# Optimization experiments

Measured on AMD Instinct MI355X. Metric: run time of the kernel, lower is better.

The kernel has to match this reference:

```python
import jax, jax.numpy as jnp
import numpy as np

B, T, E = 2, 2048, 1024
H, D = 16, 64          # num_heads, head_dim (v_head_dim == head_dim)


def setup_inputs() -> dict:
    key = jax.random.key(0)
    ks = jax.random.split(key, 10)
    s = lambda fan_in: 1.0 / np.sqrt(fan_in)
    inp = {
        "embed": jax.random.normal(ks[0], (B, T, E), dtype=jnp.float32),
        "mask": jax.random.randint(ks[1], (B, T, T), 0, 2) > 0,
        # Linear weights stored as [in, out] (y = x @ W + b)
        "Wq": jax.random.uniform(ks[2], (E, H * D), minval=-s(E), maxval=s(E)),
        "bq": jnp.zeros((H * D,), jnp.float32),
        "Wk": jax.random.uniform(ks[3], (E, H * D), minval=-s(E), maxval=s(E)),
        "bk": jnp.zeros((H * D,), jnp.float32),
        "Wv": jax.random.uniform(ks[4], (E, H * D), minval=-s(E), maxval=s(E)),
        "bv": jnp.zeros((H * D,), jnp.float32),
        "Wz": jax.random.uniform(ks[5], (H * D, E), minval=-s(H * D), maxval=s(H * D)),
        "bz": jnp.zeros((E,), jnp.float32),
    }
    return inp


def reference(embed, mask, Wq, bq, Wk, bk, Wv, bv, Wz, bz):
    # Self-attention: context = embed
    q = (embed @ Wq + bq).reshape(B, T, H, D)   # b t h d
    k = (embed @ Wk + bk).reshape(B, T, H, D)   # b T h d
    v = (embed @ Wv + bv).reshape(B, T, H, D)   # b T h d

    scale = D ** (-0.5)
    score = jnp.einsum('bthd,bThd->bhtT', q, k) * scale   # [b,h,t,T] materialized, as in source
    max_neg = -jnp.finfo(score.dtype).max
    score = jnp.where(mask[:, None, :, :], score, max_neg)
    norm_score = jax.nn.softmax(score, axis=-1)
    z = jnp.einsum('bhtT,bThd->bthd', norm_score, v)      # [b,t,h,d]
    flat_z = z.reshape(B, T, H * D)
    return flat_z @ Wz + bz
```

## Files before the change

kernel.cpp:

```cpp
#include <hip/hip_runtime.h>
#include <hip/hip_bf16.h>


typedef __bf16 bf8_t  __attribute__((ext_vector_type(8)));
typedef __bf16 bf4_t  __attribute__((ext_vector_type(4)));
typedef float  f4_t   __attribute__((ext_vector_type(4)));

constexpr int Bb = 2, Tt = 2048, Hh = 16, Dd = 64;

#define ASYNC16(g, l)                                                        \
    __builtin_amdgcn_global_load_lds(                                        \
        (const __attribute__((address_space(1))) void*)(g),                  \
        (__attribute__((address_space(3))) void*)(l), 16, 0, 0)

#if __has_builtin(__builtin_amdgcn_exp2f)
#define EXP2F(x) __builtin_amdgcn_exp2f(x)
#else
#define EXP2F(x) exp2f(x)
#endif

__global__ __launch_bounds__(256) void convert_kernel(
    const float* __restrict__ in, __bf16* __restrict__ out)
{
    int i = (blockIdx.x * 256 + threadIdx.x) * 4;
    float4 v = *reinterpret_cast<const float4*>(in + i);
    bf4_t o = {(__bf16)v.x, (__bf16)v.y, (__bf16)v.z, (__bf16)v.w};
    *reinterpret_cast<bf4_t*>(out + i) = o;
}

__global__ __launch_bounds__(256) void transpose_kernel(
    const float* __restrict__ w0, const float* __restrict__ w1,
    const float* __restrict__ w2, const float* __restrict__ w3,
    __bf16* __restrict__ o0, __bf16* __restrict__ o1,
    __bf16* __restrict__ o2, __bf16* __restrict__ o3)
{
    const float* in; __bf16* out;
    switch (blockIdx.z) {
        case 0: in = w0; out = o0; break;
        case 1: in = w1; out = o1; break;
        case 2: in = w2; out = o2; break;
        default: in = w3; out = o3; break;
    }
    __shared__ float t[32][33];
    int x  = threadIdx.x & 31;
    int y0 = threadIdx.x >> 5;
    int bx = blockIdx.x * 32;
    int by = blockIdx.y * 32;
    #pragma unroll
    for (int i = 0; i < 4; i++) {
        int y = y0 + i * 8;
        t[y][x] = in[(size_t)(by + y) * 1024 + bx + x];
    }
    __syncthreads();
    #pragma unroll
    for (int i = 0; i < 4; i++) {
        int y = y0 + i * 8;
        out[(size_t)(bx + y) * 1024 + by + x] = (__bf16)t[x][y];
    }
}

template <int TM, typename OutT>
__device__ __forceinline__ void gemm_body(const __bf16* __restrict__ A,
                                          const __bf16* __restrict__ Bt,
                                          const float* __restrict__ bias,
                                          OutT* __restrict__ out,
                                          int mode, float oscale, int bx, int by)
{
    constexpr int NI = TM / 32;
    alignas(16) __shared__ __bf16 As[TM * 64];
    alignas(16) __shared__ __bf16 Bs[128 * 64];

    int tid  = threadIdx.x;
    int lane = tid & 63;
    int quad = lane >> 4;
    int l16  = lane & 15;
    int wave = tid >> 6;
    int wm   = wave >> 1, wn = wave & 1;

    f4_t acc[NI][4];
    #pragma unroll
    for (int i = 0; i < NI; i++)
        #pragma unroll
        for (int j = 0; j < 4; j++)
            acc[i][j] = f4_t{0.f, 0.f, 0.f, 0.f};

    for (int kt = 0; kt < 1024; kt += 64) {
        #pragma unroll
        for (int i = 0; i < TM / 32; i++) {
            int c   = tid + 256 * i;
            int row = c >> 3, j = c & 7;
            ASYNC16(A + (size_t)(by * TM + row) * 1024 + kt + ((j ^ (row & 7)) * 8),
                    &As[c * 8]);
        }
        #pragma unroll
        for (int i = 0; i < 4; i++) {
            int c   = tid + 256 * i;
            int row = c >> 3, j = c & 7;
            ASYNC16(Bt + (size_t)(bx * 128 + row) * 1024 + kt + ((j ^ (row & 7)) * 8),
                    &Bs[c * 8]);
        }
        __syncthreads();

        bf8_t af[2][NI], bfr[2][4];
        #pragma unroll
        for (int c = 0; c < 2; c++) {
            #pragma unroll
            for (int im = 0; im < NI; im++) {
                int row = wm * (TM / 2) + im * 16 + l16;
                af[c][im] = *reinterpret_cast<const bf8_t*>(
                    &As[row * 64 + (((c * 4 + quad) ^ (row & 7)) * 8)]);
            }
            #pragma unroll
            for (int in_ = 0; in_ < 4; in_++) {
                int row = wn * 64 + in_ * 16 + l16;
                bfr[c][in_] = *reinterpret_cast<const bf8_t*>(
                    &Bs[row * 64 + (((c * 4 + quad) ^ (row & 7)) * 8)]);
            }
        }
        #pragma unroll
        for (int c = 0; c < 2; c++)
            #pragma unroll
            for (int im = 0; im < NI; im++)
                #pragma unroll
                for (int in_ = 0; in_ < 4; in_++)
                    acc[im][in_] = __builtin_amdgcn_mfma_f32_16x16x32_bf16(
                        af[c][im], bfr[c][in_], acc[im][in_], 0, 0, 0);
        __syncthreads();
    }

    #pragma unroll
    for (int im = 0; im < NI; im++) {
        #pragma unroll
        for (int in_ = 0; in_ < 4; in_++) {
            int gc  = bx * 128 + wn * 64 + in_ * 16 + l16;
            float bb = bias[gc];
            int gr0 = by * TM + wm * (TM / 2) + im * 16 + quad * 4;
            if (mode == 2) {
                int b = gr0 >> 11, t0 = gr0 & 2047;
                int h = gc >> 6,  d = gc & 63;
                bf4_t ov;
                #pragma unroll
                for (int r = 0; r < 4; r++)
                    ov[r] = (__bf16)(acc[im][in_][r] + bb);
                *reinterpret_cast<bf4_t*>(
                    (__bf16*)out + ((size_t)(b * Hh + h) * Dd + d) * Tt + t0) = ov;
            } else {
                #pragma unroll
                for (int r = 0; r < 4; r++) {
                    int gr  = gr0 + r;
                    float v = (acc[im][in_][r] + bb) * oscale;
                    size_t idx;
                    if (mode == 0) {
                        idx = (size_t)gr * 1024 + gc;
                    } else {
                        int b = gr >> 11, t = gr & 2047;
                        int h = gc >> 6,  d = gc & 63;
                        idx = ((size_t)(b * Hh + h) * Tt + t) * Dd + d;
                    }
                    out[idx] = (OutT)v;
                }
            }
        }
    }
}

__global__ __launch_bounds__(256) void gemm_qkv_kernel(
    const __bf16* __restrict__ A,
    const __bf16* __restrict__ WqT, const __bf16* __restrict__ WkT, const __bf16* __restrict__ WvT,
    const float* __restrict__ bq,  const float* __restrict__ bk,  const float* __restrict__ bv,
    __bf16* __restrict__ Qo, __bf16* __restrict__ Ko, __bf16* __restrict__ Vo)
{
    const __bf16* Bt; const float* bias; __bf16* out; int mode; float sc;
    if      (blockIdx.z == 0) { Bt = WqT; bias = bq; out = Qo; mode = 1; sc = 0.18033688011112042f; }
    else if (blockIdx.z == 1) { Bt = WkT; bias = bk; out = Ko; mode = 1; sc = 1.f; }
    else                      { Bt = WvT; bias = bv; out = Vo; mode = 2; sc = 1.f; }
    gemm_body<128, __bf16>(A, Bt, bias, out, mode, sc, blockIdx.x, blockIdx.y);
}

__global__ __launch_bounds__(256) void gemm_out_kernel(
    const __bf16* __restrict__ A, const __bf16* __restrict__ Bt,
    const float* __restrict__ bias, float* __restrict__ out)
{
    gemm_body<64, float>(A, Bt, bias, out, 0, 1.f, blockIdx.x, blockIdx.y);
}

__global__ __launch_bounds__(512, 4) void flash_kernel(
    const __bf16* __restrict__ Qb, const __bf16* __restrict__ Kb,
    const __bf16* __restrict__ Vb, const int* __restrict__ mask,
    __bf16* __restrict__ Zb)
{
    alignas(16) __shared__ __bf16 Ks[2][64 * 64];
    alignas(16) __shared__ __bf16 Vs[2][64 * 64];
    alignas(16) __shared__ __bf16 Ps[8 * 16 * 72];

    int tid  = threadIdx.x;
    int lane = tid & 63;
    int wave = tid >> 6;
    int quad = lane >> 4;
    int l16  = lane & 15;
    int b = blockIdx.z, h = blockIdx.y;
    int bh = b * Hh + h;
    int qrow = blockIdx.x * 128 + wave * 16;

    int srow = tid >> 3, sj = tid & 7;
    const __bf16* kgp = Kb + ((size_t)bh * Tt + srow) * Dd + ((sj ^ (srow & 7)) * 8);
    const __bf16* vgp = Vb + ((size_t)bh * Dd + srow) * Tt + ((sj ^ (srow & 7)) * 8);
    const int sdst = tid * 8;

    bf8_t qf[2];
    #pragma unroll
    for (int c = 0; c < 2; c++)
        qf[c] = *reinterpret_cast<const bf8_t*>(
            Qb + ((size_t)bh * Tt + qrow + l16) * Dd + c * 32 + quad * 8);

    const int* mp = mask + ((size_t)b * Tt + qrow + l16) * Tt + quad * 4;

    float l_i = 0.f;
    f4_t o[4];
    #pragma unroll
    for (int d = 0; d < 4; d++) o[d] = f4_t{0.f, 0.f, 0.f, 0.f};

    __bf16* pw = Ps + wave * 16 * 72;

    bf8_t kreg = *reinterpret_cast<const bf8_t*>(kgp);
    bf8_t vreg = *reinterpret_cast<const bf8_t*>(vgp);
    int4 ireg[4];
    #pragma unroll
    for (int n = 0; n < 4; n++)
        ireg[n] = *reinterpret_cast<const int4*>(mp + n * 16);

    for (int kt = 0; kt < Tt; kt += 64) {
        int par = (kt >> 6) & 1;
        *reinterpret_cast<bf8_t*>(&Ks[par][sdst]) = kreg;
        *reinterpret_cast<bf8_t*>(&Vs[par][sdst]) = vreg;
        f4_t s[4];
        #pragma unroll
        for (int n = 0; n < 4; n++)
            s[n] = f4_t{ireg[n].x ? 0.f : -1e30f, ireg[n].y ? 0.f : -1e30f,
                        ireg[n].z ? 0.f : -1e30f, ireg[n].w ? 0.f : -1e30f};
        __syncthreads();

        int ktn = (kt + 64 < Tt) ? kt + 64 : 0;
        kreg = *reinterpret_cast<const bf8_t*>(kgp + (size_t)ktn * Dd);
        vreg = *reinterpret_cast<const bf8_t*>(vgp + ktn);
        #pragma unroll
        for (int n = 0; n < 4; n++)
            ireg[n] = *reinterpret_cast<const int4*>(mp + ktn + n * 16);

        #pragma unroll
        for (int c = 0; c < 2; c++)
            #pragma unroll
            for (int n = 0; n < 4; n++) {
                int krow = n * 16 + l16;
                bf8_t kf = *reinterpret_cast<const bf8_t*>(
                    &Ks[par][krow * 64 + (((c * 4 + quad) ^ (krow & 7)) * 8)]);
                s[n] = __builtin_amdgcn_mfma_f32_16x16x32_bf16(kf, qf[c], s[n], 0, 0, 0);
            }

        float rs = 0.f;
        #pragma unroll
        for (int n = 0; n < 4; n++) {
            bf4_t pv4;
            #pragma unroll
            for (int r = 0; r < 4; r++) {
                float p = EXP2F(s[n][r]);
                rs += p;
                pv4[r] = (__bf16)p;
            }
            *reinterpret_cast<bf4_t*>(&pw[l16 * 72 + n * 16 + quad * 4]) = pv4;
        }
        rs += __shfl_xor(rs, 16);
        rs += __shfl_xor(rs, 32);
        l_i += rs;

        #pragma unroll
        for (int c = 0; c < 2; c++) {
            bf8_t pf = *reinterpret_cast<const bf8_t*>(
                &pw[l16 * 72 + c * 32 + quad * 8]);
            #pragma unroll
            for (int ds = 0; ds < 4; ds++) {
                int vrow = ds * 16 + l16;
                bf8_t vf = *reinterpret_cast<const bf8_t*>(
                    &Vs[par][vrow * 64 + (((c * 4 + quad) ^ (vrow & 7)) * 8)]);
                o[ds] = __builtin_amdgcn_mfma_f32_16x16x32_bf16(vf, pf, o[ds], 0, 0, 0);
            }
        }
    }

    float inv = 1.f / fmaxf(l_i, 1e-30f);
    size_t zrow = ((size_t)b * Tt + qrow + l16) * 1024 + h * 64;
    #pragma unroll
    for (int ds = 0; ds < 4; ds++) {
        bf4_t ov;
        #pragma unroll
        for (int r = 0; r < 4; r++) ov[r] = (__bf16)(o[ds][r] * inv);
        *reinterpret_cast<bf4_t*>(Zb + zrow + ds * 16 + quad * 4) = ov;
    }
}

extern "C" void kernel_launch(void* const* d_in, const int* in_sizes, int n_in,
                              void* d_out, int out_size, void* d_ws, size_t ws_size,
                              hipStream_t stream)
{
    (void)in_sizes; (void)n_in; (void)out_size; (void)ws_size;

    const float* embed = (const float*)d_in[0];
    const int*   mask  = (const int*)d_in[1];
    const float* Wq = (const float*)d_in[2];
    const float* bq = (const float*)d_in[3];
    const float* Wk = (const float*)d_in[4];
    const float* bk = (const float*)d_in[5];
    const float* Wv = (const float*)d_in[6];
    const float* bv = (const float*)d_in[7];
    const float* Wz = (const float*)d_in[8];
    const float* bz = (const float*)d_in[9];
    float* out = (float*)d_out;

    char* ws = (char*)d_ws;
    const size_t MB = (size_t)1024 * 1024;
    __bf16* WqT = (__bf16*)(ws + 0 * MB);
    __bf16* WkT = (__bf16*)(ws + 2 * MB);
    __bf16* WvT = (__bf16*)(ws + 4 * MB);
    __bf16* WzT = (__bf16*)(ws + 6 * MB);
    __bf16* Eb  = (__bf16*)(ws + 8 * MB);
    __bf16* Qb  = (__bf16*)(ws + 16 * MB);
    __bf16* Kb  = (__bf16*)(ws + 24 * MB);
    __bf16* Vb  = (__bf16*)(ws + 32 * MB);
    __bf16* Zb  = (__bf16*)(ws + 40 * MB);

    convert_kernel<<<dim3(4096), 256, 0, stream>>>(embed, Eb);
    transpose_kernel<<<dim3(32, 32, 4), 256, 0, stream>>>(Wq, Wk, Wv, Wz,
                                                          WqT, WkT, WvT, WzT);
    gemm_qkv_kernel<<<dim3(8, 32, 3), 256, 0, stream>>>(Eb, WqT, WkT, WvT,
                                                        bq, bk, bv, Qb, Kb, Vb);
    flash_kernel<<<dim3(16, Hh, Bb), 512, 0, stream>>>(Qb, Kb, Vb, mask, Zb);
    gemm_out_kernel<<<dim3(8, 64, 1), 256, 0, stream>>>(Zb, WzT, bz, out);
}
```

Before: 238.2 us.

## Pack attention mask into bitmask and fuse prep kernels into one launch

A single prep kernel now does the weight transposes, the embed conversion, and a new pass that packs the int32 mask into 32-bit bitmasks. The flash kernel reads 64 mask bits per row per tile instead of 64 ints. It also zeroes masked probabilities directly instead of seeding scores with -1e30, and sums the bf16-rounded probabilities. This cuts the mask traffic seen by each of the 16 heads per batch and removes one launch. The cost is an extra full pass over the mask in prep and an extra select in the softmax loop.

```diff
diff --git a/kernel.cpp b/kernel.cpp
--- a/kernel.cpp
+++ b/kernel.cpp
@@ -19,43 +19,62 @@
 #define EXP2F(x) exp2f(x)
 #endif
 
-__global__ __launch_bounds__(256) void convert_kernel(
-    const float* __restrict__ in, __bf16* __restrict__ out)
-{
-    int i = (blockIdx.x * 256 + threadIdx.x) * 4;
-    float4 v = *reinterpret_cast<const float4*>(in + i);
-    bf4_t o = {(__bf16)v.x, (__bf16)v.y, (__bf16)v.z, (__bf16)v.w};
-    *reinterpret_cast<bf4_t*>(out + i) = o;
-}
-
-__global__ __launch_bounds__(256) void transpose_kernel(
+__global__ __launch_bounds__(256) void prep_kernel(
+    const float* __restrict__ embed, const int* __restrict__ mask,
     const float* __restrict__ w0, const float* __restrict__ w1,
     const float* __restrict__ w2, const float* __restrict__ w3,
     __bf16* __restrict__ o0, __bf16* __restrict__ o1,
-    __bf16* __restrict__ o2, __bf16* __restrict__ o3)
-{
-    const float* in; __bf16* out;
-    switch (blockIdx.z) {
-        case 0: in = w0; out = o0; break;
-        case 1: in = w1; out = o1; break;
-        case 2: in = w2; out = o2; break;
-        default: in = w3; out = o3; break;
-    }
-    __shared__ float t[32][33];
-    int x  = threadIdx.x & 31;
-    int y0 = threadIdx.x >> 5;
-    int bx = blockIdx.x * 32;
-    int by = blockIdx.y * 32;
-    #pragma unroll
-    for (int i = 0; i < 4; i++) {
-        int y = y0 + i * 8;
-        t[y][x] = in[(size_t)(by + y) * 1024 + bx + x];
-    }
-    __syncthreads();
-    #pragma unroll
-    for (int i = 0; i < 4; i++) {
-        int y = y0 + i * 8;
-        out[(size_t)(bx + y) * 1024 + by + x] = (__bf16)t[x][y];
+    __bf16* __restrict__ o2, __bf16* __restrict__ o3,
+    __bf16* __restrict__ Eb, unsigned* __restrict__ Mbits)
+{
+    int z = blockIdx.x;
+    if (z < 4096) {
+        const float* in; __bf16* out;
+        switch (z >> 10) {
+            case 0: in = w0; out = o0; break;
+            case 1: in = w1; out = o1; break;
+            case 2: in = w2; out = o2; break;
+            default: in = w3; out = o3; break;
+        }
+        int rem = z & 1023;
+        int bx = (rem & 31) * 32;
+        int by = (rem >> 5) * 32;
+        __shared__ float t[32][33];
+        int x  = threadIdx.x & 31;
+        int y0 = threadIdx.x >> 5;
+        #pragma unroll
+        for (int i = 0; i < 4; i++) {
+            int y = y0 + i * 8;
+            t[y][x] = in[(size_t)(by + y) * 1024 + bx + x];
+        }
+        __syncthreads();
+        #pragma unroll
+        for (int i = 0; i < 4; i++) {
+            int y = y0 + i * 8;
+            out[(size_t)(bx + y) * 1024 + by + x] = (__bf16)t[x][y];
+        }
+    } else if (z < 5120) {
+        size_t base = (size_t)(z - 4096) * 4096;
+        #pragma unroll
+        for (int j = 0; j < 4; j++) {
+            size_t i = base + j * 1024 + threadIdx.x * 4;
+            float4 v = *reinterpret_cast<const float4*>(embed + i);
+            bf4_t o = {(__bf16)v.x, (__bf16)v.y, (__bf16)v.z, (__bf16)v.w};
+            *reinterpret_cast<bf4_t*>(Eb + i) = o;
+        }
+    } else {
+        size_t g = (size_t)(z - 5120) * 256 + threadIdx.x;
+        const int* mp = mask + g * 32;
+        unsigned v = 0;
+        #pragma unroll
+        for (int i = 0; i < 8; i++) {
+            int4 m4 = *reinterpret_cast<const int4*>(mp + i * 4);
+            if (m4.x) v |= 1u << (i * 4 + 0);
+            if (m4.y) v |= 1u << (i * 4 + 1);
+            if (m4.z) v |= 1u << (i * 4 + 2);
+            if (m4.w) v |= 1u << (i * 4 + 3);
+        }
+        Mbits[g] = v;
     }
 }
 
@@ -186,7 +205,7 @@
 
 __global__ __launch_bounds__(512, 4) void flash_kernel(
     const __bf16* __restrict__ Qb, const __bf16* __restrict__ Kb,
-    const __bf16* __restrict__ Vb, const int* __restrict__ mask,
+    const __bf16* __restrict__ Vb, const unsigned* __restrict__ Mbits,
     __bf16* __restrict__ Zb)
 {
     alignas(16) __shared__ __bf16 Ks[2][64 * 64];
@@ -213,7 +232,7 @@
         qf[c] = *reinterpret_cast<const bf8_t*>(
             Qb + ((size_t)bh * Tt + qrow + l16) * Dd + c * 32 + quad * 8);
 
-    const int* mp = mask + ((size_t)b * Tt + qrow + l16) * Tt + quad * 4;
+    const unsigned* bmp = Mbits + ((size_t)b * Tt + qrow + l16) * 64;
 
     float l_i = 0.f;
     f4_t o[4];
@@ -224,29 +243,26 @@
 
     bf8_t kreg = *reinterpret_cast<const bf8_t*>(kgp);
     bf8_t vreg = *reinterpret_cast<const bf8_t*>(vgp);
-    int4 ireg[4];
-    #pragma unroll
-    for (int n = 0; n < 4; n++)
-        ireg[n] = *reinterpret_cast<const int4*>(mp + n * 16);
+    unsigned long long mreg = *reinterpret_cast<const unsigned long long*>(bmp);
 
     for (int kt = 0; kt < Tt; kt += 64) {
         int par = (kt >> 6) & 1;
         *reinterpret_cast<bf8_t*>(&Ks[par][sdst]) = kreg;
         *reinterpret_cast<bf8_t*>(&Vs[par][sdst]) = vreg;
-        f4_t s[4];
+        unsigned nib[4];
         #pragma unroll
         for (int n = 0; n < 4; n++)
-            s[n] = f4_t{ireg[n].x ? 0.f : -1e30f, ireg[n].y ? 0.f : -1e30f,
-                        ireg[n].z ? 0.f : -1e30f, ireg[n].w ? 0.f : -1e30f};
+            nib[n] = (unsigned)(mreg >> (n * 16 + quad * 4)) & 0xFu;
         __syncthreads();
 
         int ktn = (kt + 64 < Tt) ? kt + 64 : 0;
         kreg = *reinterpret_cast<const bf8_t*>(kgp + (size_t)ktn * Dd);
         vreg = *reinterpret_cast<const bf8_t*>(vgp + ktn);
-        #pragma unroll
-        for (int n = 0; n < 4; n++)
-            ireg[n] = *reinterpret_cast<const int4*>(mp + ktn + n * 16);
-
+        mreg = *reinterpret_cast<const unsigned long long*>(bmp + (ktn >> 5));
+
+        f4_t s[4];
+        #pragma unroll
+        for (int n = 0; n < 4; n++) s[n] = f4_t{0.f, 0.f, 0.f, 0.f};
         #pragma unroll
         for (int c = 0; c < 2; c++)
             #pragma unroll
@@ -263,9 +279,10 @@
             bf4_t pv4;
             #pragma unroll
             for (int r = 0; r < 4; r++) {
-                float p = EXP2F(s[n][r]);
-                rs += p;
-                pv4[r] = (__bf16)p;
+                float p = (nib[n] & (1u << r)) ? EXP2F(s[n][r]) : 0.f;
+                __bf16 pb = (__bf16)p;
+                rs += (float)pb;
+                pv4[r] = pb;
             }
             *reinterpret_cast<bf4_t*>(&pw[l16 * 72 + n * 16 + quad * 4]) = pv4;
         }
@@ -318,21 +335,21 @@
 
     char* ws = (char*)d_ws;
     const size_t MB = (size_t)1024 * 1024;
-    __bf16* WqT = (__bf16*)(ws + 0 * MB);
-    __bf16* WkT = (__bf16*)(ws + 2 * MB);
-    __bf16* WvT = (__bf16*)(ws + 4 * MB);
-    __bf16* WzT = (__bf16*)(ws + 6 * MB);
-    __bf16* Eb  = (__bf16*)(ws + 8 * MB);
-    __bf16* Qb  = (__bf16*)(ws + 16 * MB);
-    __bf16* Kb  = (__bf16*)(ws + 24 * MB);
-    __bf16* Vb  = (__bf16*)(ws + 32 * MB);
-    __bf16* Zb  = (__bf16*)(ws + 40 * MB);
-
-    convert_kernel<<<dim3(4096), 256, 0, stream>>>(embed, Eb);
-    transpose_kernel<<<dim3(32, 32, 4), 256, 0, stream>>>(Wq, Wk, Wv, Wz,
-                                                          WqT, WkT, WvT, WzT);
+    __bf16*   WqT = (__bf16*)(ws + 0 * MB);
+    __bf16*   WkT = (__bf16*)(ws + 2 * MB);
+    __bf16*   WvT = (__bf16*)(ws + 4 * MB);
+    __bf16*   WzT = (__bf16*)(ws + 6 * MB);
+    __bf16*   Eb  = (__bf16*)(ws + 8 * MB);
+    __bf16*   Qb  = (__bf16*)(ws + 16 * MB);
+    __bf16*   Kb  = (__bf16*)(ws + 24 * MB);
+    __bf16*   Vb  = (__bf16*)(ws + 32 * MB);
+    __bf16*   Zb  = (__bf16*)(ws + 40 * MB);
+    unsigned* Mb  = (unsigned*)(ws + 48 * MB);
+
+    prep_kernel<<<dim3(6144), 256, 0, stream>>>(embed, mask, Wq, Wk, Wv, Wz,
+                                                WqT, WkT, WvT, WzT, Eb, Mb);
     gemm_qkv_kernel<<<dim3(8, 32, 3), 256, 0, stream>>>(Eb, WqT, WkT, WvT,
                                                         bq, bk, bv, Qb, Kb, Vb);
-    flash_kernel<<<dim3(16, Hh, Bb), 512, 0, stream>>>(Qb, Kb, Vb, mask, Zb);
+    flash_kernel<<<dim3(16, Hh, Bb), 512, 0, stream>>>(Qb, Kb, Vb, Mb, Zb);
     gemm_out_kernel<<<dim3(8, 64, 1), 256, 0, stream>>>(Zb, WzT, bz, out);
 }
```

After: 231.4 us. 1.03x faster.
